# Kernel optimization log

Hardware: AMD Instinct MI355X
Metric: run time of the kernel (lower is better)

The kernel has to match this reference:

```python
import jax, jax.numpy as jnp
import numpy as np

N, D, K = 10000, 784, 16          # nodes, input feat dim, num_neighbors
E = N * (K - 1)                   # edges
H = 128                           # hidden width in all MLPs
SIZES = [784, 128, 2]             # node_sizes


def setup_inputs() -> dict:
    key = jax.random.key(0)
    ks = jax.random.split(key, 24)
    w = lambda k, shape: jax.random.normal(k, shape, jnp.float32) * 0.02
    inp = {
        "x": jax.random.normal(ks[0], (N, D), jnp.float32),
        "edge_attr": jax.random.uniform(ks[1], (E, 1), jnp.float32),
        "idxs": jax.random.randint(ks[2], (N, K - 1), 0, N, dtype=jnp.int32),
    }
    # Layer 1: in=784, msg_size=784, out=128
    inp["l1_msg_w1"] = w(ks[3], (D + 1, H));      inp["l1_msg_b1"] = jnp.zeros((H,), jnp.float32)
    inp["l1_msg_w2"] = w(ks[4], (H, D));          inp["l1_msg_b2"] = jnp.zeros((D,), jnp.float32)
    inp["l1_node_w1"] = w(ks[5], (D + D, H));     inp["l1_node_b1"] = jnp.zeros((H,), jnp.float32)
    inp["l1_node_w2"] = w(ks[6], (H, 128));       inp["l1_node_b2"] = jnp.zeros((128,), jnp.float32)
    # Layer 2: in=128, msg_size=128, out=2
    inp["l2_msg_w1"] = w(ks[7], (128 + 1, H));    inp["l2_msg_b1"] = jnp.zeros((H,), jnp.float32)
    inp["l2_msg_w2"] = w(ks[8], (H, 128));        inp["l2_msg_b2"] = jnp.zeros((128,), jnp.float32)
    inp["l2_node_w1"] = w(ks[9], (128 + 128, H)); inp["l2_node_b1"] = jnp.zeros((H,), jnp.float32)
    inp["l2_node_w2"] = w(ks[10], (H, 2));        inp["l2_node_b2"] = jnp.zeros((2,), jnp.float32)
    return inp


def _mlp(x, w1, b1, w2, b2):
    return jax.nn.relu(x @ w1 + b1) @ w2 + b2


def _node_layer(x, src, edge_attr,
                mw1, mb1, mw2, mb2, nw1, nb1, nw2, nb2):
    # message over edges: cat(x[src], edge_attr) -> MLP   [E, msg_size]
    msg = _mlp(jnp.concatenate([x[src], edge_attr], axis=1), mw1, mb1, mw2, mb2)
    # scatter_mean by src index (faithful to the original, which uses index=src)
    sums = jax.ops.segment_sum(msg, src, num_segments=N)
    cnt = jax.ops.segment_sum(jnp.ones((src.shape[0], 1), msg.dtype), src, num_segments=N)
    agg = jnp.where(cnt > 0, sums / jnp.maximum(cnt, 1.0), 0.0)
    # node update: cat(x, agg_msg) -> MLP
    return _mlp(jnp.concatenate([x, agg], axis=1), nw1, nb1, nw2, nb2)


def reference(x, edge_attr, idxs,
              l1_msg_w1, l1_msg_b1, l1_msg_w2, l1_msg_b2,
              l1_node_w1, l1_node_b1, l1_node_w2, l1_node_b2,
              l2_msg_w1, l2_msg_b1, l2_msg_w2, l2_msg_b2,
              l2_node_w1, l2_node_b1, l2_node_w2, l2_node_b2):
    src = idxs.reshape(-1)  # [E]; dst is unused by the original message computation
    h = _node_layer(x, src, edge_attr,
                    l1_msg_w1, l1_msg_b1, l1_msg_w2, l1_msg_b2,
                    l1_node_w1, l1_node_b1, l1_node_w2, l1_node_b2)
    proj = _node_layer(h, src, edge_attr,
                       l2_msg_w1, l2_msg_b1, l2_msg_w2, l2_msg_b2,
                       l2_node_w1, l2_node_b1, l2_node_w2, l2_node_b2)  # [N, 2]
    # vectorized per-neighbor squared distances (replaces the nested python loop)
    neigh = proj[idxs]                                   # [N, K-1, 2]
    d = jnp.sum((proj[:, None, :] - neigh) ** 2, axis=-1)  # [N, K-1]
    return d.reshape(-1, 1)                              # [N*(K-1), 1]
```

## Files before the change

### kernel.cpp

```cpp
#include <hip/hip_runtime.h>

#define N_NODES 10000
#define E_EDGES 150000
#define KNB     15
#define EBLOCKS 587
#define GEMM_BLOCKS 628

__global__ void count_kernel(const int* __restrict__ idxs, int* __restrict__ cnt, int e) {
    int i = blockIdx.x * blockDim.x + threadIdx.x;
    if (i < e) atomicAdd(&cnt[idxs[i]], 1);
}

__device__ __forceinline__
void gemm_tile2(const float* __restrict__ A, int K,
                const float* __restrict__ Blo, const float* __restrict__ Bhi, int ldB,
                float* __restrict__ C, int ldC, int M,
                int rowBlk, int colBlk) {
    __shared__ float As2[16][34];
    __shared__ float Bs2[16][64];
    int tid = threadIdx.x;
    int tn  = tid & 15, tm = tid >> 4;
    int arow = tid >> 3, acB = (tid & 7) << 1;
    int brow = tid >> 4, bcol = (tid & 15) << 2;
    int rowBase = rowBlk * 32, colBase = colBlk * 64;

    bool half = (Bhi != nullptr) && (colBase >= 128);
    const float* B = half ? Bhi : Blo;
    int bj = colBase - (half ? 128 : 0) + bcol;

    float2 av; float4 bv;
    auto loadA = [&](int k0, float2& dst) {
        int gr = rowBase + arow;
        if (gr < M) dst = *(const float2*)(A + (size_t)gr * K + k0 + acB);
        else { dst.x = dst.y = 0.f; }
    };
    auto loadB = [&](int k0, float4& dst) {
        dst = *(const float4*)(B + (size_t)(k0 + brow) * ldB + bj);
    };
    loadA(0, av); loadB(0, bv);

    float acc[2][4] = {};
    for (int k0 = 0; k0 < K; k0 += 16) {
        __syncthreads();
        As2[acB + 0][arow] = av.x; As2[acB + 1][arow] = av.y;
        *(float4*)&Bs2[brow][bcol] = bv;
        __syncthreads();
        if (k0 + 16 < K) { loadA(k0 + 16, av); loadB(k0 + 16, bv); }
#pragma unroll
        for (int k = 0; k < 16; ++k) {
            float4 b = *(const float4*)&Bs2[k][tn << 2];
            float2 a = *(const float2*)&As2[k][tm << 1];
            acc[0][0] = fmaf(a.x, b.x, acc[0][0]); acc[0][1] = fmaf(a.x, b.y, acc[0][1]);
            acc[0][2] = fmaf(a.x, b.z, acc[0][2]); acc[0][3] = fmaf(a.x, b.w, acc[0][3]);
            acc[1][0] = fmaf(a.y, b.x, acc[1][0]); acc[1][1] = fmaf(a.y, b.y, acc[1][1]);
            acc[1][2] = fmaf(a.y, b.z, acc[1][2]); acc[1][3] = fmaf(a.y, b.w, acc[1][3]);
        }
    }
#pragma unroll
    for (int i = 0; i < 2; ++i) {
        int row = rowBase + tm * 2 + i;
        if (row >= M) continue;
#pragma unroll
        for (int j = 0; j < 4; ++j)
            C[(size_t)row * ldC + colBase + (tn << 2) + j] = acc[i][j];
    }
}

__global__ __launch_bounds__(256)
void scanfold_kernel(const float* __restrict__ mw2, const float* __restrict__ mb2,
                     const float* __restrict__ nw1, const float* __restrict__ nb2,
                     const float* __restrict__ nw2,
                     const float* __restrict__ m2w1, const float* __restrict__ m2b1,
                     const float* __restrict__ m2w2, const float* __restrict__ m2b2,
                     const float* __restrict__ n2w1, const float* __restrict__ n2b1,
                     float* __restrict__ M1, float* __restrict__ M2,
                     float* __restrict__ WH,
                     float* __restrict__ v1, float* __restrict__ v2,
                     float* __restrict__ bu2, float* __restrict__ bx2,
                     const int* __restrict__ cnt, int* __restrict__ eoff,
                     float* __restrict__ maskv, int* __restrict__ fillc) {
    int b = blockIdx.x;
    if (b == 0) {
        __shared__ int ssum[256];
        int tid = threadIdx.x;
        const int CH = 40;
        int base = tid * CH;
        int v[CH]; int s = 0;
#pragma unroll
        for (int q = 0; q < CH; ++q) {
            int i = base + q;
            v[q] = (i < N_NODES) ? cnt[i] : 0;
            s += v[q];
        }
        ssum[tid] = s;
        __syncthreads();
        for (int off = 1; off < 256; off <<= 1) {
            int t = (tid >= off) ? ssum[tid - off] : 0;
            __syncthreads();
            ssum[tid] += t;
            __syncthreads();
        }
        int ex = ssum[tid] - s;
#pragma unroll
        for (int q = 0; q < CH; ++q) {
            int i = base + q;
            if (i < N_NODES) {
                eoff[i]  = ex;
                maskv[i] = (v[q] > 0) ? 1.f : 0.f;
                fillc[i] = 0;
                ex += v[q];
            }
        }
        return;
    }
    b -= 1;
    if (b < 8) {
        gemm_tile2(mw2, 784, nw1 + 784 * 128, nullptr, 128, M1, 128, 128, b >> 1, b & 1);
    } else if (b < 16) {
        int t = b - 8;
        gemm_tile2(m2w2, 128, n2w1 + 128 * 128, nullptr, 128, M2, 128, 128, t >> 1, t & 1);
    } else if (b < 32) {
        int t = b - 16;
        gemm_tile2(nw2, 128, m2w1, n2w1, 128, WH, 256, 128, t >> 2, t & 3);
    } else {
        __shared__ float red[256];
        int t  = (b - 32) >> 1;
        int j  = ((b - 32) & 1) * 64 + (threadIdx.x & 63);
        int kq = threadIdx.x >> 6;
        const float* bvec; const float* Bv; const float* add; float* out; int Kv;
        if (t == 0)      { bvec = mb2;  Bv = nw1 + 784 * 128;  add = nullptr; out = v1;  Kv = 784; }
        else if (t == 1) { bvec = m2b2; Bv = n2w1 + 128 * 128; add = nullptr; out = v2;  Kv = 128; }
        else if (t == 2) { bvec = nb2;  Bv = m2w1;             add = m2b1;    out = bu2; Kv = 128; }
        else             { bvec = nb2;  Bv = n2w1;             add = n2b1;    out = bx2; Kv = 128; }
        float acc = 0.f;
        for (int k = kq; k < Kv; k += 4) acc = fmaf(bvec[k], Bv[k * 128 + j], acc);
        red[threadIdx.x] = acc;
        __syncthreads();
        if (threadIdx.x < 64) {
            float tot = red[threadIdx.x] + red[threadIdx.x + 64] +
                        red[threadIdx.x + 128] + red[threadIdx.x + 192];
            out[j] = tot + (add ? add[j] : 0.f);
        }
    }
}

__device__ __forceinline__
void gemm784_tile(const float* __restrict__ A,
                  const float* __restrict__ B0, const float* __restrict__ B1,
                  const float* __restrict__ biasLo, const float* __restrict__ biasHi,
                  const float* __restrict__ vhi, const float* __restrict__ rowmask,
                  float* __restrict__ C, int M, int gb) {
    __shared__ float As[16][68];
    __shared__ float Bs[16][64];
    int rb = gb >> 2, cb = gb & 3;
    int tid = threadIdx.x;
    int tm = tid >> 4, tn = tid & 15;
    int arow = tid >> 2, ac4 = (tid & 3) << 2;
    int brow = tid >> 4, bc4 = (tid & 15) << 2;
    int rowBase = rb * 64, colBase = cb * 64;
    bool hi = colBase >= 128;
    const float* B    = hi ? B1 : B0;
    const float* bias = hi ? biasHi : biasLo;
    int bj = ((cb & 1) << 6) + bc4;

    int gr = rowBase + arow; if (gr > M - 1) gr = M - 1;
    const float* Ap = A + (size_t)gr * 784;

    float4 av, bv;
    av = *(const float4*)(Ap + ac4);
    bv = *(const float4*)(B + (size_t)brow * 128 + bj);

    float acc[4][4] = {};
    for (int k0 = 0; k0 < 784; k0 += 16) {
        __syncthreads();
        As[ac4 + 0][arow] = av.x;
        As[ac4 + 1][arow] = av.y;
        As[ac4 + 2][arow] = av.z;
        As[ac4 + 3][arow] = av.w;
        *(float4*)&Bs[brow][bc4] = bv;
        __syncthreads();
        if (k0 + 16 < 784) {
            av = *(const float4*)(Ap + k0 + 16 + ac4);
            bv = *(const float4*)(B + (size_t)(k0 + 16 + brow) * 128 + bj);
        }
#pragma unroll
        for (int k = 0; k < 16; ++k) {
            float4 a = *(const float4*)&As[k][tm << 2];
            float4 b = *(const float4*)&Bs[k][tn << 2];
            acc[0][0] = fmaf(a.x, b.x, acc[0][0]); acc[0][1] = fmaf(a.x, b.y, acc[0][1]);
            acc[0][2] = fmaf(a.x, b.z, acc[0][2]); acc[0][3] = fmaf(a.x, b.w, acc[0][3]);
            acc[1][0] = fmaf(a.y, b.x, acc[1][0]); acc[1][1] = fmaf(a.y, b.y, acc[1][1]);
            acc[1][2] = fmaf(a.y, b.z, acc[1][2]); acc[1][3] = fmaf(a.y, b.w, acc[1][3]);
            acc[2][0] = fmaf(a.z, b.x, acc[2][0]); acc[2][1] = fmaf(a.z, b.y, acc[2][1]);
            acc[2][2] = fmaf(a.z, b.z, acc[2][2]); acc[2][3] = fmaf(a.z, b.w, acc[2][3]);
            acc[3][0] = fmaf(a.w, b.x, acc[3][0]); acc[3][1] = fmaf(a.w, b.y, acc[3][1]);
            acc[3][2] = fmaf(a.w, b.z, acc[3][2]); acc[3][3] = fmaf(a.w, b.w, acc[3][3]);
        }
    }

#pragma unroll
    for (int i = 0; i < 4; ++i) {
        int row = rowBase + (tm << 2) + i;
        if (row >= M) continue;
        float rm = hi ? rowmask[row] : 0.f;
#pragma unroll
        for (int j = 0; j < 4; ++j) {
            int gcol = colBase + (tn << 2) + j;
            int cj   = gcol & 127;
            float v = acc[i][j] + bias[cj];
            if (hi) v = fmaf(rm, vhi[cj], v);
            C[(size_t)row * 256 + gcol] = v;
        }
    }
}

__global__ __launch_bounds__(256)
void fillgemm_kernel(const int* __restrict__ idxs, const float* __restrict__ ea,
                     const int* __restrict__ eoff, int* __restrict__ fillc,
                     float* __restrict__ eas,
                     const float* __restrict__ A,
                     const float* __restrict__ B0, const float* __restrict__ B1,
                     const float* __restrict__ biasLo, const float* __restrict__ biasHi,
                     const float* __restrict__ vhi, const float* __restrict__ rowmask,
                     float* __restrict__ C, int M) {
    int gb = blockIdx.x;
    if (gb < EBLOCKS) {
        int i = gb * 256 + threadIdx.x;
        if (i < E_EDGES) {
            int s = idxs[i];
            int p = atomicAdd(&fillc[s], 1);
            eas[eoff[s] + p] = ea[i];
        }
        return;
    }
    gemm784_tile(A, B0, B1, biasLo, biasHi, vhi, rowmask, C, M, gb - EBLOCKS);
}

__global__ __launch_bounds__(256)
void tail16_kernel(const float* __restrict__ UX1, const float* __restrict__ w1last,
                   const float* __restrict__ eas, const int* __restrict__ eoff,
                   const int* __restrict__ cnt, const float* __restrict__ maskv,
                   const float* __restrict__ M1, const float* __restrict__ WH,
                   const float* __restrict__ bu2, const float* __restrict__ bx2,
                   const float* __restrict__ v2,
                   const float* __restrict__ w2last, const float* __restrict__ M2,
                   const float* __restrict__ pw, const float* __restrict__ pb,
                   float* __restrict__ UX2, float* __restrict__ proj) {
    __shared__ float Bs[16][264];
    __shared__ float mhT[128][18];
    __shared__ float ts[16][132];
    __shared__ float ebuf[1024];
    int rowBase = blockIdx.x * 16;
    int tid = threadIdx.x;
    int tm2 = tid >> 5;
    int tn  = tid & 31;

    auto msg_phase = [&](const float* __restrict__ U, const float* __restrict__ wl) {
        int d = tid & 127, sub = tid >> 7;
        float w = wl[d];
        float uu[8], sum[8];
        int es[8], ec[8];
#pragma unroll
        for (int it = 0; it < 8; ++it) {
            int n  = rowBase + it * 2 + sub;
            ec[it] = cnt[n];
            es[it] = eoff[n];
            uu[it] = U[(size_t)n * 256 + d];
            sum[it] = 0.f;
        }
        int ebase = eoff[rowBase];
        int eend  = (rowBase + 16 < N_NODES) ? eoff[rowBase + 16] : E_EDGES;
        for (int w0 = ebase; w0 < eend; w0 += 1024) {
            int wlen = min(1024, eend - w0);
            __syncthreads();
            for (int q = tid; q < wlen; q += 256) ebuf[q] = eas[w0 + q];
            __syncthreads();
#pragma unroll
            for (int it = 0; it < 8; ++it) {
                int lo = max(es[it], w0), hiE = min(es[it] + ec[it], w0 + wlen);
                for (int e = lo; e < hiE; ++e)
                    sum[it] += fmaxf(fmaf(ebuf[e - w0], w, uu[it]), 0.f);
            }
        }
#pragma unroll
        for (int it = 0; it < 8; ++it)
            mhT[d][it * 2 + sub] = (ec[it] > 0) ? sum[it] / (float)ec[it] : 0.f;
    };

    msg_phase(UX1, w1last);
    __syncthreads();

    {
        float acc[2][4] = {};
        for (int k0 = 0; k0 < 128; k0 += 16) {
            int kr = tid >> 4, c8 = (tid & 15) << 3;
            *(float4*)&Bs[kr][c8]     = *(const float4*)(M1 + (size_t)(k0 + kr) * 128 + c8);
            *(float4*)&Bs[kr][c8 + 4] = *(const float4*)(M1 + (size_t)(k0 + kr) * 128 + c8 + 4);
            __syncthreads();
#pragma unroll
            for (int k = 0; k < 16; ++k) {
                float2 a = *(const float2*)&mhT[k0 + k][tm2 << 1];
                float4 b = *(const float4*)&Bs[k][tn << 2];
                acc[0][0] = fmaf(a.x, b.x, acc[0][0]); acc[0][1] = fmaf(a.x, b.y, acc[0][1]);
                acc[0][2] = fmaf(a.x, b.z, acc[0][2]); acc[0][3] = fmaf(a.x, b.w, acc[0][3]);
                acc[1][0] = fmaf(a.y, b.x, acc[1][0]); acc[1][1] = fmaf(a.y, b.y, acc[1][1]);
                acc[1][2] = fmaf(a.y, b.z, acc[1][2]); acc[1][3] = fmaf(a.y, b.w, acc[1][3]);
            }
            __syncthreads();
        }
#pragma unroll
        for (int i = 0; i < 2; ++i) {
            int row = rowBase + (tm2 << 1) + i;
            float4 xn = *(const float4*)(UX1 + (size_t)row * 256 + 128 + (tn << 2));
            float4 o;
            o.x = fmaxf(acc[i][0] + xn.x, 0.f);
            o.y = fmaxf(acc[i][1] + xn.y, 0.f);
            o.z = fmaxf(acc[i][2] + xn.z, 0.f);
            o.w = fmaxf(acc[i][3] + xn.w, 0.f);
            *(float4*)&ts[(tm2 << 1) + i][tn << 2] = o;
        }
    }

    {
        float acc[2][8] = {};
        for (int k0 = 0; k0 < 128; k0 += 16) {
            int kr = tid >> 4, c4 = (tid & 15) << 2;
#pragma unroll
            for (int p = 0; p < 4; ++p)
                *(float4*)&Bs[kr][c4 + p * 64] =
                    *(const float4*)(WH + (size_t)(k0 + kr) * 256 + c4 + p * 64);
            __syncthreads();
#pragma unroll
            for (int k = 0; k < 16; ++k) {
                float4 b0 = *(const float4*)&Bs[k][tn << 3];
                float4 b1 = *(const float4*)&Bs[k][(tn << 3) + 4];
                float br[8] = {b0.x, b0.y, b0.z, b0.w, b1.x, b1.y, b1.z, b1.w};
#pragma unroll
                for (int i = 0; i < 2; ++i) {
                    float a = ts[(tm2 << 1) + i][k0 + k];
#pragma unroll
                    for (int j = 0; j < 8; ++j)
                        acc[i][j] = fmaf(a, br[j], acc[i][j]);
                }
            }
            __syncthreads();
        }
        bool hi = tn >= 16;
        const float* bias = hi ? bx2 : bu2;
#pragma unroll
        for (int i = 0; i < 2; ++i) {
            int row = rowBase + (tm2 << 1) + i;
            float rm = maskv[row];
            float4 o0, o1; float* po0 = (float*)&o0; float* po1 = (float*)&o1;
#pragma unroll
            for (int j = 0; j < 4; ++j) {
                int cj0 = ((tn << 3) + j) & 127, cj1 = ((tn << 3) + 4 + j) & 127;
                float q0 = acc[i][j]     + bias[cj0];
                float q1 = acc[i][4 + j] + bias[cj1];
                if (hi) { q0 = fmaf(rm, v2[cj0], q0); q1 = fmaf(rm, v2[cj1], q1); }
                po0[j] = q0; po1[j] = q1;
            }
            float* orow = UX2 + (size_t)row * 256 + (tn << 3);
            *(float4*)orow       = o0;
            *(float4*)(orow + 4) = o1;
        }
    }
    __syncthreads();

    msg_phase(UX2, w2last);

    {
        float acc[2][4] = {};
        for (int k0 = 0; k0 < 128; k0 += 16) {
            int kr = tid >> 4, c8 = (tid & 15) << 3;
            *(float4*)&Bs[kr][c8]     = *(const float4*)(M2 + (size_t)(k0 + kr) * 128 + c8);
            *(float4*)&Bs[kr][c8 + 4] = *(const float4*)(M2 + (size_t)(k0 + kr) * 128 + c8 + 4);
            __syncthreads();
#pragma unroll
            for (int k = 0; k < 16; ++k) {
                float2 a = *(const float2*)&mhT[k0 + k][tm2 << 1];
                float4 b = *(const float4*)&Bs[k][tn << 2];
                acc[0][0] = fmaf(a.x, b.x, acc[0][0]); acc[0][1] = fmaf(a.x, b.y, acc[0][1]);
                acc[0][2] = fmaf(a.x, b.z, acc[0][2]); acc[0][3] = fmaf(a.x, b.w, acc[0][3]);
                acc[1][0] = fmaf(a.y, b.x, acc[1][0]); acc[1][1] = fmaf(a.y, b.y, acc[1][1]);
                acc[1][2] = fmaf(a.y, b.z, acc[1][2]); acc[1][3] = fmaf(a.y, b.w, acc[1][3]);
            }
            __syncthreads();
        }
        float pp0[2], pp1[2];
#pragma unroll
        for (int i = 0; i < 2; ++i) {
            int row = rowBase + (tm2 << 1) + i;
            float4 xn = *(const float4*)(UX2 + (size_t)row * 256 + 128 + (tn << 2));
            float t0 = fmaxf(acc[i][0] + xn.x, 0.f);
            float t1 = fmaxf(acc[i][1] + xn.y, 0.f);
            float t2 = fmaxf(acc[i][2] + xn.z, 0.f);
            float t3 = fmaxf(acc[i][3] + xn.w, 0.f);
            int c = tn << 2;
            pp0[i] = fmaf(t3, pw[2*(c+3)],   fmaf(t2, pw[2*(c+2)],   fmaf(t1, pw[2*(c+1)],   t0 * pw[2*c])));
            pp1[i] = fmaf(t3, pw[2*(c+3)+1], fmaf(t2, pw[2*(c+2)+1], fmaf(t1, pw[2*(c+1)+1], t0 * pw[2*c+1])));
        }
        for (int off = 16; off > 0; off >>= 1) {
            pp0[0] += __shfl_xor(pp0[0], off, 64);
            pp0[1] += __shfl_xor(pp0[1], off, 64);
            pp1[0] += __shfl_xor(pp1[0], off, 64);
            pp1[1] += __shfl_xor(pp1[1], off, 64);
        }
        if (tn == 0) {
#pragma unroll
            for (int i = 0; i < 2; ++i) {
                int row = rowBase + (tm2 << 1) + i;
                proj[2 * row]     = pp0[i] + pb[0];
                proj[2 * row + 1] = pp1[i] + pb[1];
            }
        }
    }
}

__global__ void dist_kernel(const float* __restrict__ proj, const int* __restrict__ idxs,
                            float* __restrict__ out, int e) {
    int i = blockIdx.x * blockDim.x + threadIdx.x;
    if (i >= e) return;
    int n = i / KNB;
    int m = idxs[i];
    float2 pn = *(const float2*)(proj + 2 * n);
    float2 pm = *(const float2*)(proj + 2 * m);
    float dx = pn.x - pm.x;
    float dy = pn.y - pm.y;
    out[i] = dx * dx + dy * dy;
}

extern "C" void kernel_launch(void* const* d_in, const int* in_sizes, int n_in,
                              void* d_out, int out_size, void* d_ws, size_t ws_size,
                              hipStream_t stream) {
    (void)in_sizes; (void)n_in; (void)out_size; (void)ws_size;
    const float* x    = (const float*)d_in[0];
    const float* eatt = (const float*)d_in[1];
    const int*   idxs = (const int*)d_in[2];
    const float* mw1  = (const float*)d_in[3];
    const float* mb1  = (const float*)d_in[4];
    const float* mw2  = (const float*)d_in[5];
    const float* mb2  = (const float*)d_in[6];
    const float* nw1  = (const float*)d_in[7];
    const float* nb1  = (const float*)d_in[8];
    const float* nw2  = (const float*)d_in[9];
    const float* nb2  = (const float*)d_in[10];
    const float* m2w1 = (const float*)d_in[11];
    const float* m2b1 = (const float*)d_in[12];
    const float* m2w2 = (const float*)d_in[13];
    const float* m2b2 = (const float*)d_in[14];
    const float* n2w1 = (const float*)d_in[15];
    const float* n2b1 = (const float*)d_in[16];
    const float* n2w2 = (const float*)d_in[17];
    const float* n2b2 = (const float*)d_in[18];
    float* out = (float*)d_out;

    float* fws   = (float*)d_ws;
    float* UX1   = fws;
    float* UX2   = fws + 2560000;
    float* proj  = fws + 5120000;
    float* maskv = fws + 5140000;
    float* eas   = fws + 5150016;
    float* M1    = fws + 5300016;
    float* M2    = fws + 5316400;
    float* WH    = fws + 5332784;
    float* v1    = fws + 5365552;
    float* v2    = fws + 5365680;
    float* bu2   = fws + 5365808;
    float* bx2   = fws + 5365936;
    int*   cnt   = (int*)(fws + 5366064);
    int*   fillc = cnt + N_NODES;
    int*   eoff  = fillc + N_NODES;

    hipMemsetAsync(cnt, 0, N_NODES * sizeof(int), stream);
    count_kernel<<<EBLOCKS, 256, 0, stream>>>(idxs, cnt, E_EDGES);

    scanfold_kernel<<<41, 256, 0, stream>>>(mw2, mb2, nw1, nb2, nw2,
                                            m2w1, m2b1, m2w2, m2b2, n2w1, n2b1,
                                            M1, M2, WH, v1, v2, bu2, bx2,
                                            cnt, eoff, maskv, fillc);

    fillgemm_kernel<<<EBLOCKS + GEMM_BLOCKS, 256, 0, stream>>>(
        idxs, eatt, eoff, fillc, eas,
        x, mw1, nw1, mb1, nb1, v1, maskv, UX1, N_NODES);

    tail16_kernel<<<625, 256, 0, stream>>>(UX1, mw1 + 784 * 128, eas, eoff, cnt, maskv,
                                           M1, WH, bu2, bx2, v2,
                                           m2w1 + 128 * 128, M2,
                                           n2w2, n2b2,
                                           UX2, proj);

    dist_kernel<<<EBLOCKS, 256, 0, stream>>>(proj, idxs, out, E_EDGES);
}
```

Baseline: 302.7 us.

## Fuse edge counting with weight folding and register-prefetch B tiles in tail GEMMs

Edge-degree counting now runs in the same launch as the weight-folding GEMMs, and the prefix scan moves to its own single-block kernel. Kernel count stays the same, but the weight folding no longer waits behind the count kernel. In tail16's three small GEMM loops, the next B tile is loaded into registers while the current tile is being computed, and the barrier placement is rearranged. This adds register pressure and an extra barrier per iteration; the fold and count blocks now share one grid.

```diff
diff --git a/kernel.cpp b/kernel.cpp
--- a/kernel.cpp
+++ b/kernel.cpp
@@ -5,11 +5,6 @@
 #define KNB     15
 #define EBLOCKS 587
 #define GEMM_BLOCKS 628
-
-__global__ void count_kernel(const int* __restrict__ idxs, int* __restrict__ cnt, int e) {
-    int i = blockIdx.x * blockDim.x + threadIdx.x;
-    if (i < e) atomicAdd(&cnt[idxs[i]], 1);
-}
 
 __device__ __forceinline__
 void gemm_tile2(const float* __restrict__ A, int K,
@@ -67,53 +62,24 @@
 }
 
 __global__ __launch_bounds__(256)
-void scanfold_kernel(const float* __restrict__ mw2, const float* __restrict__ mb2,
-                     const float* __restrict__ nw1, const float* __restrict__ nb2,
-                     const float* __restrict__ nw2,
-                     const float* __restrict__ m2w1, const float* __restrict__ m2b1,
-                     const float* __restrict__ m2w2, const float* __restrict__ m2b2,
-                     const float* __restrict__ n2w1, const float* __restrict__ n2b1,
-                     float* __restrict__ M1, float* __restrict__ M2,
-                     float* __restrict__ WH,
-                     float* __restrict__ v1, float* __restrict__ v2,
-                     float* __restrict__ bu2, float* __restrict__ bx2,
-                     const int* __restrict__ cnt, int* __restrict__ eoff,
-                     float* __restrict__ maskv, int* __restrict__ fillc) {
+void countfold_kernel(const int* __restrict__ idxs, int* __restrict__ cnt,
+                      const float* __restrict__ mw2, const float* __restrict__ mb2,
+                      const float* __restrict__ nw1, const float* __restrict__ nb2,
+                      const float* __restrict__ nw2,
+                      const float* __restrict__ m2w1, const float* __restrict__ m2b1,
+                      const float* __restrict__ m2w2, const float* __restrict__ m2b2,
+                      const float* __restrict__ n2w1, const float* __restrict__ n2b1,
+                      float* __restrict__ M1, float* __restrict__ M2,
+                      float* __restrict__ WH,
+                      float* __restrict__ v1, float* __restrict__ v2,
+                      float* __restrict__ bu2, float* __restrict__ bx2) {
     int b = blockIdx.x;
-    if (b == 0) {
-        __shared__ int ssum[256];
-        int tid = threadIdx.x;
-        const int CH = 40;
-        int base = tid * CH;
-        int v[CH]; int s = 0;
-#pragma unroll
-        for (int q = 0; q < CH; ++q) {
-            int i = base + q;
-            v[q] = (i < N_NODES) ? cnt[i] : 0;
-            s += v[q];
-        }
-        ssum[tid] = s;
-        __syncthreads();
-        for (int off = 1; off < 256; off <<= 1) {
-            int t = (tid >= off) ? ssum[tid - off] : 0;
-            __syncthreads();
-            ssum[tid] += t;
-            __syncthreads();
-        }
-        int ex = ssum[tid] - s;
-#pragma unroll
-        for (int q = 0; q < CH; ++q) {
-            int i = base + q;
-            if (i < N_NODES) {
-                eoff[i]  = ex;
-                maskv[i] = (v[q] > 0) ? 1.f : 0.f;
-                fillc[i] = 0;
-                ex += v[q];
-            }
-        }
+    if (b < EBLOCKS) {
+        int i = b * 256 + threadIdx.x;
+        if (i < E_EDGES) atomicAdd(&cnt[idxs[i]], 1);
         return;
     }
-    b -= 1;
+    b -= EBLOCKS;
     if (b < 8) {
         gemm_tile2(mw2, 784, nw1 + 784 * 128, nullptr, 128, M1, 128, 128, b >> 1, b & 1);
     } else if (b < 16) {
@@ -144,6 +110,41 @@
     }
 }
 
+__global__ __launch_bounds__(256)
+void scan_kernel(const int* __restrict__ cnt, int* __restrict__ eoff,
+                 float* __restrict__ maskv, int* __restrict__ fillc) {
+    __shared__ int ssum[256];
+    int tid = threadIdx.x;
+    const int CH = 40;
+    int base = tid * CH;
+    int v[CH]; int s = 0;
+#pragma unroll
+    for (int q = 0; q < CH; ++q) {
+        int i = base + q;
+        v[q] = (i < N_NODES) ? cnt[i] : 0;
+        s += v[q];
+    }
+    ssum[tid] = s;
+    __syncthreads();
+    for (int off = 1; off < 256; off <<= 1) {
+        int t = (tid >= off) ? ssum[tid - off] : 0;
+        __syncthreads();
+        ssum[tid] += t;
+        __syncthreads();
+    }
+    int ex = ssum[tid] - s;
+#pragma unroll
+    for (int q = 0; q < CH; ++q) {
+        int i = base + q;
+        if (i < N_NODES) {
+            eoff[i]  = ex;
+            maskv[i] = (v[q] > 0) ? 1.f : 0.f;
+            fillc[i] = 0;
+            ex += v[q];
+        }
+    }
+}
+
 __device__ __forceinline__
 void gemm784_tile(const float* __restrict__ A,
                   const float* __restrict__ B0, const float* __restrict__ B1,
@@ -288,15 +289,21 @@
     };
 
     msg_phase(UX1, w1last);
-    __syncthreads();
 
     {
+        int kr = tid >> 4, c8 = (tid & 15) << 3;
+        float4 pf0 = *(const float4*)(M1 + (size_t)kr * 128 + c8);
+        float4 pf1 = *(const float4*)(M1 + (size_t)kr * 128 + c8 + 4);
         float acc[2][4] = {};
         for (int k0 = 0; k0 < 128; k0 += 16) {
-            int kr = tid >> 4, c8 = (tid & 15) << 3;
-            *(float4*)&Bs[kr][c8]     = *(const float4*)(M1 + (size_t)(k0 + kr) * 128 + c8);
-            *(float4*)&Bs[kr][c8 + 4] = *(const float4*)(M1 + (size_t)(k0 + kr) * 128 + c8 + 4);
-            __syncthreads();
+            __syncthreads();
+            *(float4*)&Bs[kr][c8]     = pf0;
+            *(float4*)&Bs[kr][c8 + 4] = pf1;
+            __syncthreads();
+            if (k0 + 16 < 128) {
+                pf0 = *(const float4*)(M1 + (size_t)(k0 + 16 + kr) * 128 + c8);
+                pf1 = *(const float4*)(M1 + (size_t)(k0 + 16 + kr) * 128 + c8 + 4);
+            }
 #pragma unroll
             for (int k = 0; k < 16; ++k) {
                 float2 a = *(const float2*)&mhT[k0 + k][tm2 << 1];
@@ -306,8 +313,8 @@
                 acc[1][0] = fmaf(a.y, b.x, acc[1][0]); acc[1][1] = fmaf(a.y, b.y, acc[1][1]);
                 acc[1][2] = fmaf(a.y, b.z, acc[1][2]); acc[1][3] = fmaf(a.y, b.w, acc[1][3]);
             }
-            __syncthreads();
-        }
+        }
+        __syncthreads();
 #pragma unroll
         for (int i = 0; i < 2; ++i) {
             int row = rowBase + (tm2 << 1) + i;
@@ -322,14 +329,23 @@
     }
 
     {
+        int kr = tid >> 4, c4 = (tid & 15) << 2;
+        float4 pf[4];
+#pragma unroll
+        for (int p = 0; p < 4; ++p)
+            pf[p] = *(const float4*)(WH + (size_t)kr * 256 + c4 + p * 64);
         float acc[2][8] = {};
         for (int k0 = 0; k0 < 128; k0 += 16) {
-            int kr = tid >> 4, c4 = (tid & 15) << 2;
+            __syncthreads();
 #pragma unroll
             for (int p = 0; p < 4; ++p)
-                *(float4*)&Bs[kr][c4 + p * 64] =
-                    *(const float4*)(WH + (size_t)(k0 + kr) * 256 + c4 + p * 64);
-            __syncthreads();
+                *(float4*)&Bs[kr][c4 + p * 64] = pf[p];
+            __syncthreads();
+            if (k0 + 16 < 128) {
+#pragma unroll
+                for (int p = 0; p < 4; ++p)
+                    pf[p] = *(const float4*)(WH + (size_t)(k0 + 16 + kr) * 256 + c4 + p * 64);
+            }
 #pragma unroll
             for (int k = 0; k < 16; ++k) {
                 float4 b0 = *(const float4*)&Bs[k][tn << 3];
@@ -343,7 +359,6 @@
                         acc[i][j] = fmaf(a, br[j], acc[i][j]);
                 }
             }
-            __syncthreads();
         }
         bool hi = tn >= 16;
         const float* bias = hi ? bx2 : bu2;
@@ -370,12 +385,19 @@
     msg_phase(UX2, w2last);
 
     {
+        int kr = tid >> 4, c8 = (tid & 15) << 3;
+        float4 pf0 = *(const float4*)(M2 + (size_t)kr * 128 + c8);
+        float4 pf1 = *(const float4*)(M2 + (size_t)kr * 128 + c8 + 4);
         float acc[2][4] = {};
         for (int k0 = 0; k0 < 128; k0 += 16) {
-            int kr = tid >> 4, c8 = (tid & 15) << 3;
-            *(float4*)&Bs[kr][c8]     = *(const float4*)(M2 + (size_t)(k0 + kr) * 128 + c8);
-            *(float4*)&Bs[kr][c8 + 4] = *(const float4*)(M2 + (size_t)(k0 + kr) * 128 + c8 + 4);
-            __syncthreads();
+            __syncthreads();
+            *(float4*)&Bs[kr][c8]     = pf0;
+            *(float4*)&Bs[kr][c8 + 4] = pf1;
+            __syncthreads();
+            if (k0 + 16 < 128) {
+                pf0 = *(const float4*)(M2 + (size_t)(k0 + 16 + kr) * 128 + c8);
+                pf1 = *(const float4*)(M2 + (size_t)(k0 + 16 + kr) * 128 + c8 + 4);
+            }
 #pragma unroll
             for (int k = 0; k < 16; ++k) {
                 float2 a = *(const float2*)&mhT[k0 + k][tm2 << 1];
@@ -385,7 +407,6 @@
                 acc[1][0] = fmaf(a.y, b.x, acc[1][0]); acc[1][1] = fmaf(a.y, b.y, acc[1][1]);
                 acc[1][2] = fmaf(a.y, b.z, acc[1][2]); acc[1][3] = fmaf(a.y, b.w, acc[1][3]);
             }
-            __syncthreads();
         }
         float pp0[2], pp1[2];
 #pragma unroll
@@ -473,12 +494,13 @@
     int*   eoff  = fillc + N_NODES;
 
     hipMemsetAsync(cnt, 0, N_NODES * sizeof(int), stream);
-    count_kernel<<<EBLOCKS, 256, 0, stream>>>(idxs, cnt, E_EDGES);
-
-    scanfold_kernel<<<41, 256, 0, stream>>>(mw2, mb2, nw1, nb2, nw2,
-                                            m2w1, m2b1, m2w2, m2b2, n2w1, n2b1,
-                                            M1, M2, WH, v1, v2, bu2, bx2,
-                                            cnt, eoff, maskv, fillc);
+    countfold_kernel<<<EBLOCKS + 40, 256, 0, stream>>>(
+        idxs, cnt,
+        mw2, mb2, nw1, nb2, nw2,
+        m2w1, m2b1, m2w2, m2b2, n2w1, n2b1,
+        M1, M2, WH, v1, v2, bu2, bx2);
+
+    scan_kernel<<<1, 256, 0, stream>>>(cnt, eoff, maskv, fillc);
 
     fillgemm_kernel<<<EBLOCKS + GEMM_BLOCKS, 256, 0, stream>>>(
         idxs, eatt, eoff, fillc, eas,
```

Result: slower. 330.5 us (+9.2%).

## Redistribute weight-fold work across count and fill kernels to shorten scan stage

Applied to the files above, without the earlier changes.

The weight-folding work (the small GEMMs M1/M2/WH and the bias vectors) moves out of the scan kernel. The v1 fold now runs alongside the edge counting kernel, and the other folds run as extra blocks of the fill/GEMM kernel. The scan kernel becomes a single block. This takes the slow 784-deep fold GEMM off the serial path between counting and filling, and overlaps it with concurrent work. The cost is a bigger fused kernel whose extra blocks may finish late, plus more shared-memory declarations in the merged kernel, which could lower occupancy.

```diff
diff --git a/kernel.cpp b/kernel.cpp
--- a/kernel.cpp
+++ b/kernel.cpp
@@ -5,11 +5,6 @@
 #define KNB     15
 #define EBLOCKS 587
 #define GEMM_BLOCKS 628
-
-__global__ void count_kernel(const int* __restrict__ idxs, int* __restrict__ cnt, int e) {
-    int i = blockIdx.x * blockDim.x + threadIdx.x;
-    if (i < e) atomicAdd(&cnt[idxs[i]], 1);
-}
 
 __device__ __forceinline__
 void gemm_tile2(const float* __restrict__ A, int K,
@@ -66,80 +61,67 @@
     }
 }
 
+__device__ __forceinline__
+void vrow_task(const float* __restrict__ bvec, const float* __restrict__ Bv, int Kv,
+               const float* __restrict__ add, float* __restrict__ out, int jhalf) {
+    __shared__ float red[256];
+    int j  = jhalf * 64 + (threadIdx.x & 63);
+    int kq = threadIdx.x >> 6;
+    float acc = 0.f;
+    for (int k = kq; k < Kv; k += 4) acc = fmaf(bvec[k], Bv[k * 128 + j], acc);
+    red[threadIdx.x] = acc;
+    __syncthreads();
+    if (threadIdx.x < 64) {
+        float tot = red[threadIdx.x] + red[threadIdx.x + 64] +
+                    red[threadIdx.x + 128] + red[threadIdx.x + 192];
+        out[j] = tot + (add ? add[j] : 0.f);
+    }
+}
+
 __global__ __launch_bounds__(256)
-void scanfold_kernel(const float* __restrict__ mw2, const float* __restrict__ mb2,
-                     const float* __restrict__ nw1, const float* __restrict__ nb2,
-                     const float* __restrict__ nw2,
-                     const float* __restrict__ m2w1, const float* __restrict__ m2b1,
-                     const float* __restrict__ m2w2, const float* __restrict__ m2b2,
-                     const float* __restrict__ n2w1, const float* __restrict__ n2b1,
-                     float* __restrict__ M1, float* __restrict__ M2,
-                     float* __restrict__ WH,
-                     float* __restrict__ v1, float* __restrict__ v2,
-                     float* __restrict__ bu2, float* __restrict__ bx2,
-                     const int* __restrict__ cnt, int* __restrict__ eoff,
-                     float* __restrict__ maskv, int* __restrict__ fillc) {
+void countfold_kernel(const int* __restrict__ idxs, int* __restrict__ cnt,
+                      const float* __restrict__ mb2, const float* __restrict__ nw1,
+                      float* __restrict__ v1) {
     int b = blockIdx.x;
-    if (b == 0) {
-        __shared__ int ssum[256];
-        int tid = threadIdx.x;
-        const int CH = 40;
-        int base = tid * CH;
-        int v[CH]; int s = 0;
-#pragma unroll
-        for (int q = 0; q < CH; ++q) {
-            int i = base + q;
-            v[q] = (i < N_NODES) ? cnt[i] : 0;
-            s += v[q];
-        }
-        ssum[tid] = s;
+    if (b < EBLOCKS) {
+        int i = b * 256 + threadIdx.x;
+        if (i < E_EDGES) atomicAdd(&cnt[idxs[i]], 1);
+        return;
+    }
+    vrow_task(mb2, nw1 + 784 * 128, 784, nullptr, v1, b - EBLOCKS);
+}
+
+__global__ __launch_bounds__(256)
+void scan_kernel(const int* __restrict__ cnt, int* __restrict__ eoff,
+                 float* __restrict__ maskv, int* __restrict__ fillc) {
+    __shared__ int ssum[256];
+    int tid = threadIdx.x;
+    const int CH = 40;
+    int base = tid * CH;
+    int v[CH]; int s = 0;
+#pragma unroll
+    for (int q = 0; q < CH; ++q) {
+        int i = base + q;
+        v[q] = (i < N_NODES) ? cnt[i] : 0;
+        s += v[q];
+    }
+    ssum[tid] = s;
+    __syncthreads();
+    for (int off = 1; off < 256; off <<= 1) {
+        int t = (tid >= off) ? ssum[tid - off] : 0;
         __syncthreads();
-        for (int off = 1; off < 256; off <<= 1) {
-            int t = (tid >= off) ? ssum[tid - off] : 0;
-            __syncthreads();
-            ssum[tid] += t;
-            __syncthreads();
-        }
-        int ex = ssum[tid] - s;
-#pragma unroll
-        for (int q = 0; q < CH; ++q) {
-            int i = base + q;
-            if (i < N_NODES) {
-                eoff[i]  = ex;
-                maskv[i] = (v[q] > 0) ? 1.f : 0.f;
-                fillc[i] = 0;
-                ex += v[q];
-            }
-        }
-        return;
-    }
-    b -= 1;
-    if (b < 8) {
-        gemm_tile2(mw2, 784, nw1 + 784 * 128, nullptr, 128, M1, 128, 128, b >> 1, b & 1);
-    } else if (b < 16) {
-        int t = b - 8;
-        gemm_tile2(m2w2, 128, n2w1 + 128 * 128, nullptr, 128, M2, 128, 128, t >> 1, t & 1);
-    } else if (b < 32) {
-        int t = b - 16;
-        gemm_tile2(nw2, 128, m2w1, n2w1, 128, WH, 256, 128, t >> 2, t & 3);
-    } else {
-        __shared__ float red[256];
-        int t  = (b - 32) >> 1;
-        int j  = ((b - 32) & 1) * 64 + (threadIdx.x & 63);
-        int kq = threadIdx.x >> 6;
-        const float* bvec; const float* Bv; const float* add; float* out; int Kv;
-        if (t == 0)      { bvec = mb2;  Bv = nw1 + 784 * 128;  add = nullptr; out = v1;  Kv = 784; }
-        else if (t == 1) { bvec = m2b2; Bv = n2w1 + 128 * 128; add = nullptr; out = v2;  Kv = 128; }
-        else if (t == 2) { bvec = nb2;  Bv = m2w1;             add = m2b1;    out = bu2; Kv = 128; }
-        else             { bvec = nb2;  Bv = n2w1;             add = n2b1;    out = bx2; Kv = 128; }
-        float acc = 0.f;
-        for (int k = kq; k < Kv; k += 4) acc = fmaf(bvec[k], Bv[k * 128 + j], acc);
-        red[threadIdx.x] = acc;
+        ssum[tid] += t;
         __syncthreads();
-        if (threadIdx.x < 64) {
-            float tot = red[threadIdx.x] + red[threadIdx.x + 64] +
-                        red[threadIdx.x + 128] + red[threadIdx.x + 192];
-            out[j] = tot + (add ? add[j] : 0.f);
+    }
+    int ex = ssum[tid] - s;
+#pragma unroll
+    for (int q = 0; q < CH; ++q) {
+        int i = base + q;
+        if (i < N_NODES) {
+            eoff[i]  = ex;
+            maskv[i] = (v[q] > 0) ? 1.f : 0.f;
+            fillc[i] = 0;
+            ex += v[q];
         }
     }
 }
@@ -222,7 +204,16 @@
                      const float* __restrict__ B0, const float* __restrict__ B1,
                      const float* __restrict__ biasLo, const float* __restrict__ biasHi,
                      const float* __restrict__ vhi, const float* __restrict__ rowmask,
-                     float* __restrict__ C, int M) {
+                     float* __restrict__ C, int M,
+                     const float* __restrict__ mw2, const float* __restrict__ nw1,
+                     const float* __restrict__ nb2, const float* __restrict__ nw2,
+                     const float* __restrict__ m2w1, const float* __restrict__ m2b1,
+                     const float* __restrict__ m2w2, const float* __restrict__ m2b2,
+                     const float* __restrict__ n2w1, const float* __restrict__ n2b1,
+                     float* __restrict__ M1, float* __restrict__ M2,
+                     float* __restrict__ WH,
+                     float* __restrict__ v2, float* __restrict__ bu2,
+                     float* __restrict__ bx2) {
     int gb = blockIdx.x;
     if (gb < EBLOCKS) {
         int i = gb * 256 + threadIdx.x;
@@ -233,7 +224,27 @@
         }
         return;
     }
-    gemm784_tile(A, B0, B1, biasLo, biasHi, vhi, rowmask, C, M, gb - EBLOCKS);
+    gb -= EBLOCKS;
+    if (gb < GEMM_BLOCKS) {
+        gemm784_tile(A, B0, B1, biasLo, biasHi, vhi, rowmask, C, M, gb);
+        return;
+    }
+    int b = gb - GEMM_BLOCKS;
+    if (b < 8) {
+        gemm_tile2(mw2, 784, nw1 + 784 * 128, nullptr, 128, M1, 128, 128, b >> 1, b & 1);
+    } else if (b < 16) {
+        int t = b - 8;
+        gemm_tile2(m2w2, 128, n2w1 + 128 * 128, nullptr, 128, M2, 128, 128, t >> 1, t & 1);
+    } else if (b < 32) {
+        int t = b - 16;
+        gemm_tile2(nw2, 128, m2w1, n2w1, 128, WH, 256, 128, t >> 2, t & 3);
+    } else {
+        int t = (b - 32) >> 1;
+        int jh = (b - 32) & 1;
+        if (t == 0)      vrow_task(m2b2, n2w1 + 128 * 128, 128, nullptr, v2,  jh);
+        else if (t == 1) vrow_task(nb2,  m2w1,             128, m2b1,    bu2, jh);
+        else             vrow_task(nb2,  n2w1,             128, n2b1,    bx2, jh);
+    }
 }
 
 __global__ __launch_bounds__(256)
@@ -473,16 +484,15 @@
     int*   eoff  = fillc + N_NODES;
 
     hipMemsetAsync(cnt, 0, N_NODES * sizeof(int), stream);
-    count_kernel<<<EBLOCKS, 256, 0, stream>>>(idxs, cnt, E_EDGES);
-
-    scanfold_kernel<<<41, 256, 0, stream>>>(mw2, mb2, nw1, nb2, nw2,
-                                            m2w1, m2b1, m2w2, m2b2, n2w1, n2b1,
-                                            M1, M2, WH, v1, v2, bu2, bx2,
-                                            cnt, eoff, maskv, fillc);
-
-    fillgemm_kernel<<<EBLOCKS + GEMM_BLOCKS, 256, 0, stream>>>(
+    countfold_kernel<<<EBLOCKS + 2, 256, 0, stream>>>(idxs, cnt, mb2, nw1, v1);
+
+    scan_kernel<<<1, 256, 0, stream>>>(cnt, eoff, maskv, fillc);
+
+    fillgemm_kernel<<<EBLOCKS + GEMM_BLOCKS + 38, 256, 0, stream>>>(
         idxs, eatt, eoff, fillc, eas,
-        x, mw1, nw1, mb1, nb1, v1, maskv, UX1, N_NODES);
+        x, mw1, nw1, mb1, nb1, v1, maskv, UX1, N_NODES,
+        mw2, nw1, nb2, nw2, m2w1, m2b1, m2w2, m2b2, n2w1, n2b1,
+        M1, M2, WH, v2, bu2, bx2);
 
     tail16_kernel<<<625, 256, 0, stream>>>(UX1, mw1 + 784 * 128, eas, eoff, cnt, maskv,
                                            M1, WH, bu2, bx2, v2,
```

New measurement: 347.7 us. +14.9%, slower.
